# Optimization experiments

Measured on AMD Instinct MI355X. Metric: run time of the kernel, lower is better.

The kernel has to match this reference:

```python
import jax, jax.numpy as jnp
import numpy as np

B, N, P = 16, 128, 4096          # images, proposals/img, pairs/img
D_IN, D_HID = 1024, 512          # input_dim, hidden_dim
D_GEO, D_EMB = 128, 200          # geometry_feat_dim, embed_dim
N_OBJ, N_REL = 151, 51           # obj classes, rel classes (out_dim = 50)
OUT = N_REL - 1
LN_EPS = 1e-5


def _ln(x, g, b):
    mu = jnp.mean(x, axis=-1, keepdims=True)
    var = jnp.var(x, axis=-1, keepdims=True)
    return (x - mu) * jax.lax.rsqrt(var + LN_EPS) * g + b


def setup_inputs() -> dict:
    key = jax.random.key(0)
    ks = jax.random.split(key, 20)
    w = lambda k, shape: (jax.random.normal(k, shape, jnp.float32) * 0.02)
    return {
        'visual_feat': jax.random.normal(ks[0], (B * P, D_IN), jnp.float32),
        'box_info': jax.random.uniform(ks[1], (B, N, 9), jnp.float32),
        'pred_logits': jax.random.normal(ks[2], (B, N, N_OBJ), jnp.float32),
        'pair_idx': jax.random.randint(ks[3], (B, P, 2), 0, N, jnp.int32),
        'obj_sem_w': w(ks[4], (N_OBJ, D_EMB)),
        'pos_w1': w(ks[5], (9, D_GEO)), 'pos_b1': jnp.zeros((D_GEO,), jnp.float32),
        'pos_w2': w(ks[6], (D_GEO, D_GEO)), 'pos_b2': jnp.zeros((D_GEO,), jnp.float32),
        'vis_w': w(ks[7], (D_IN, D_HID)), 'vis_b': jnp.zeros((D_HID,), jnp.float32),
        'geo_w': w(ks[8], (2 * D_EMB + 2 * D_GEO, D_HID)), 'geo_b': jnp.zeros((D_HID,), jnp.float32),
        'fus_g': jnp.ones((2 * D_HID,), jnp.float32), 'fus_bt': jnp.zeros((2 * D_HID,), jnp.float32),
        'fus_w': w(ks[9], (2 * D_HID, D_HID)), 'fus_b': jnp.zeros((D_HID,), jnp.float32),
        'cls_g': jnp.ones((D_HID,), jnp.float32), 'cls_bt': jnp.zeros((D_HID,), jnp.float32),
        'cls_w': w(ks[10], (D_HID, OUT)), 'cls_b': jnp.zeros((OUT,), jnp.float32),
    }


def reference(visual_feat, box_info, pred_logits, pair_idx,
              obj_sem_w, pos_w1, pos_b1, pos_w2, pos_b2,
              vis_w, vis_b, geo_w, geo_b,
              fus_g, fus_bt, fus_w, fus_b,
              cls_g, cls_bt, cls_w, cls_b):
    # detach() in torch -> stop_gradient
    vf = jax.lax.stop_gradient(visual_feat)
    pl = jax.lax.stop_gradient(pred_logits)
    # vis_embed = Sequential(ReLU, Linear): [B*P, D_IN] -> [B, P, D_HID]
    vis = (jnp.maximum(vf, 0.0) @ vis_w + vis_b).reshape(B, P, D_HID)
    # obj_pos_embed = Linear, ReLU, Linear: [B, N, 9] -> [B, N, D_GEO]
    pos = jnp.maximum(box_info @ pos_w1 + pos_b1, 0.0) @ pos_w2 + pos_b2
    # semantic embed: softmax over obj classes @ embedding table -> [B, N, D_EMB]
    sem = jax.nn.softmax(pl, axis=-1) @ obj_sem_w
    bidx = jnp.arange(B)[:, None]
    s, o = pair_idx[..., 0], pair_idx[..., 1]
    # gather pair reps: [B, P, 2*(D_GEO+D_EMB)]
    rep = jnp.concatenate([pos[bidx, s], sem[bidx, s], pos[bidx, o], sem[bidx, o]], axis=-1)
    # proposal_box_feat_extract = Sequential(ReLU, Linear)
    geo = jnp.maximum(rep, 0.0) @ geo_w + geo_b
    # proposal_feat_fusion = Sequential(LayerNorm, ReLU, Linear)
    fused = jnp.concatenate([vis, geo], axis=-1)
    fused = jnp.maximum(_ln(fused, fus_g, fus_bt), 0.0) @ fus_w + fus_b
    # proposal_relness_cls_fc = Sequential(LayerNorm, ReLU, Linear)
    logits = jnp.maximum(_ln(fused, cls_g, cls_bt), 0.0) @ cls_w + cls_b  # [B, P, OUT]
    # predictor_type == 'single': scatter max sigmoid score into NxN matrix
    scores = jnp.max(jax.nn.sigmoid(logits), axis=-1)  # [B, P]
    rel_mat = jnp.zeros((B, N, N), logits.dtype).at[bidx, s, o].set(scores)
    return logits.reshape(B * P, OUT), rel_mat
```

## Files before the change

kernel.cpp:

```cpp
#include <hip/hip_runtime.h>
#include <cstdint>

#define B_    16
#define N_    128
#define P_    4096
#define M_    65536
#define DIN   1024
#define DHID  512
#define DGEO  128
#define DEMB  200
#define NODEF 328
#define NOBJ  151
#define OUTC  50
#define KGEO  656
#define KGEOP 672

typedef __attribute__((ext_vector_type(8))) short bf16x8;
typedef __attribute__((ext_vector_type(4))) float f32x4;

typedef __attribute__((address_space(3))) unsigned char lds_u8;
typedef __attribute__((address_space(1))) unsigned char glb_u8;

static __device__ __forceinline__ void async_copy16(const void* g, void* l) {
  __builtin_amdgcn_global_load_lds((const glb_u8*)g, (lds_u8*)l, 16, 0, 0);
}

static __device__ __forceinline__ unsigned short f2b(float f) {
  union { float f; unsigned u; } v; v.f = f;
  unsigned r = v.u + 0x7fffu + ((v.u >> 16) & 1u);
  return (unsigned short)(r >> 16);
}
static __device__ __forceinline__ float b2f(unsigned short b) {
  union { unsigned u; float f; } v; v.u = ((unsigned)b) << 16;
  return v.f;
}
static __device__ __forceinline__ unsigned pack2(float a, float b) {
  return (unsigned)f2b(a) | ((unsigned)f2b(b) << 16);
}
static __device__ __forceinline__ void unpack8(uint4 raw, float* x) {
  x[0] = b2f(raw.x & 0xffffu); x[1] = b2f(raw.x >> 16);
  x[2] = b2f(raw.y & 0xffffu); x[3] = b2f(raw.y >> 16);
  x[4] = b2f(raw.z & 0xffffu); x[5] = b2f(raw.z >> 16);
  x[6] = b2f(raw.w & 0xffffu); x[7] = b2f(raw.w >> 16);
}

#define ZN   131072
#define TV   (512 * 1024)
#define TG   (512 * KGEOP)
#define TF   (512 * 1024)
#define TC   (128 * 512)
#define PREP_TOT (ZN + TV + TG + TF + TC)
__global__ __launch_bounds__(256)
void prep_kernel(uint4* __restrict__ scat,
                 const float* __restrict__ vis_w, unsigned short* __restrict__ wT_vis,
                 const float* __restrict__ geo_w, unsigned short* __restrict__ wT_geo,
                 const float* __restrict__ fus_w, unsigned short* __restrict__ wT_fus,
                 const float* __restrict__ cls_w, unsigned short* __restrict__ wT_cls) {
  int idx = blockIdx.x * 256 + threadIdx.x;
  if (idx < ZN) { scat[idx] = make_uint4(0, 0, 0, 0); return; }
  idx -= ZN;
  if (idx < TV) {
    int n = idx >> 10, k = idx & 1023;
    wT_vis[idx] = f2b(vis_w[(size_t)k * 512 + n]);
    return;
  }
  idx -= TV;
  if (idx < TG) {
    int n = idx / KGEOP, k = idx - n * KGEOP;
    wT_geo[idx] = (k < KGEO) ? f2b(geo_w[(size_t)k * 512 + n]) : 0;
    return;
  }
  idx -= TG;
  if (idx < TF) {
    int n = idx >> 10, k = idx & 1023;
    wT_fus[idx] = f2b(fus_w[(size_t)k * 512 + n]);
    return;
  }
  idx -= TF;
  if (idx < TC) {
    int n = idx >> 9, k = idx & 511;
    wT_cls[idx] = (n < OUTC) ? f2b(cls_w[(size_t)k * OUTC + n]) : 0;
  }
}

__global__ __launch_bounds__(128)
void node_kernel(const float* __restrict__ box, const float* __restrict__ plog,
                 const float* __restrict__ semw,
                 const float* __restrict__ w1, const float* __restrict__ b1,
                 const float* __restrict__ w2, const float* __restrict__ b2,
                 unsigned short* __restrict__ nodeFb) {
  const int node = blockIdx.x;
  const int t = threadIdx.x;
  __shared__ float sBox[9];
  __shared__ float sH[128];
  __shared__ float sE[NOBJ];
  __shared__ float sRed[4];
  if (t < 9) sBox[t] = box[node * 9 + t];
  float l0 = (t < NOBJ) ? plog[node * NOBJ + t] : -1e30f;
  float l1 = (t + 128 < NOBJ) ? plog[node * NOBJ + t + 128] : -1e30f;
  __syncthreads();
  float h = b1[t];
#pragma unroll
  for (int i = 0; i < 9; i++) h = fmaf(sBox[i], w1[i * 128 + t], h);
  h = fmaxf(h, 0.f);
  sH[t] = h;
  float mx = fmaxf(l0, l1);
#pragma unroll
  for (int off = 32; off >= 1; off >>= 1) mx = fmaxf(mx, __shfl_xor(mx, off));
  if ((t & 63) == 0) sRed[t >> 6] = mx;
  __syncthreads();
  mx = fmaxf(sRed[0], sRed[1]);
  float e0 = (t < NOBJ) ? expf(l0 - mx) : 0.f;
  float e1 = (t + 128 < NOBJ) ? expf(l1 - mx) : 0.f;
  if (t < NOBJ) sE[t] = e0;
  if (t + 128 < NOBJ) sE[t + 128] = e1;
  float sm = e0 + e1;
#pragma unroll
  for (int off = 32; off >= 1; off >>= 1) sm += __shfl_xor(sm, off);
  if ((t & 63) == 0) sRed[2 + (t >> 6)] = sm;
  __syncthreads();
  const float inv = 1.f / (sRed[2] + sRed[3]);
  float pv = b2[t];
  for (int i = 0; i < 128; i++) pv = fmaf(sH[i], w2[i * 128 + t], pv);
  nodeFb[(size_t)node * NODEF + t] = f2b(fmaxf(pv, 0.f));
  float a0 = 0.f, a1 = 0.f;
  const int d1 = (t + 128 < DEMB) ? (t + 128) : 0;
  for (int i = 0; i < NOBJ; i++) {
    float e = sE[i];
    a0 = fmaf(e, semw[i * DEMB + t], a0);
    a1 = fmaf(e, semw[i * DEMB + d1], a1);
  }
  nodeFb[(size_t)node * NODEF + 128 + t] = f2b(fmaxf(a0 * inv, 0.f));
  if (t + 128 < DEMB) nodeFb[(size_t)node * NODEF + 128 + t + 128] = f2b(fmaxf(a1 * inv, 0.f));
}

template<int D>
__global__ __launch_bounds__(256)
void ln_relu_kernel(unsigned short* __restrict__ X,
                    const float* __restrict__ g, const float* __restrict__ bta) {
  constexpr int C = D / 64;
  const int lane = threadIdx.x & 63, wv = threadIdx.x >> 6;
  const size_t row = (size_t)blockIdx.x * 4 + wv;
  unsigned short* xp = X + row * D + lane * C;
  float x[C];
#pragma unroll
  for (int c = 0; c < C; c += 8) {
    uint4 raw = *(const uint4*)(xp + c);
    unpack8(raw, x + c);
  }
  float s = 0.f, s2 = 0.f;
#pragma unroll
  for (int q = 0; q < C; q++) { s += x[q]; s2 = fmaf(x[q], x[q], s2); }
#pragma unroll
  for (int off = 32; off >= 1; off >>= 1) { s += __shfl_xor(s, off); s2 += __shfl_xor(s2, off); }
  const float mu = s / D;
  const float rs = rsqrtf(s2 / D - mu * mu + 1e-5f);
  const float* gp = g + lane * C;
  const float* bp = bta + lane * C;
#pragma unroll
  for (int c = 0; c < C; c += 8) {
    float4 g0 = *(const float4*)(gp + c), g1 = *(const float4*)(gp + c + 4);
    float4 t0 = *(const float4*)(bp + c), t1 = *(const float4*)(bp + c + 4);
    float y0 = fmaxf(fmaf((x[c + 0] - mu) * rs, g0.x, t0.x), 0.f);
    float y1 = fmaxf(fmaf((x[c + 1] - mu) * rs, g0.y, t0.y), 0.f);
    float y2 = fmaxf(fmaf((x[c + 2] - mu) * rs, g0.z, t0.z), 0.f);
    float y3 = fmaxf(fmaf((x[c + 3] - mu) * rs, g0.w, t0.w), 0.f);
    float y4 = fmaxf(fmaf((x[c + 4] - mu) * rs, g1.x, t1.x), 0.f);
    float y5 = fmaxf(fmaf((x[c + 5] - mu) * rs, g1.y, t1.y), 0.f);
    float y6 = fmaxf(fmaf((x[c + 6] - mu) * rs, g1.z, t1.z), 0.f);
    float y7 = fmaxf(fmaf((x[c + 7] - mu) * rs, g1.w, t1.w), 0.f);
    uint4 u;
    u.x = pack2(y0, y1); u.y = pack2(y2, y3);
    u.z = pack2(y4, y5); u.w = pack2(y6, y7);
    *(uint4*)(xp + c) = u;
  }
}

static __device__ __forceinline__ int pair_swz(int bid, int nwg) {
  const int cpx2 = nwg >> 4;
  const int pr = bid >> 1, q = bid & 1;
  return (((pr & 7) * cpx2) + (pr >> 3)) * 2 + q;
}

template<int MODE>
__global__ __launch_bounds__(512)
void gemm256r(const unsigned short* __restrict__ A, int ldaE,
              const unsigned short* __restrict__ Bt, int ldbE,
              const float* __restrict__ bias,
              unsigned short* __restrict__ C, int ldcE, int ccol0,
              int NS, int NBN,
              const int* __restrict__ pidx,
              const unsigned short* __restrict__ nodeFb,
              const unsigned short* __restrict__ zsrc) {
  __shared__ __align__(16) unsigned char smem[131072];
  const int tid = threadIdx.x;
  const int lane = tid & 63, w = tid >> 6;
  const int swz = pair_swz(blockIdx.x, gridDim.x);
  const int bm = swz / NBN, bn = swz - bm * NBN;

  const int sslot = (tid & 3) ^ ((tid >> 3) & 3);
  const int srow = tid >> 2;
  const size_t ldaBy = (size_t)ldaE * 2, ldbBy = (size_t)ldbE * 2;
  const unsigned char* aG = (const unsigned char*)A + (size_t)(bm * 256 + srow) * ldaBy + sslot * 16;
  const unsigned char* bG = (const unsigned char*)Bt + (size_t)(bn * 256 + srow) * ldbBy + sslot * 16;

  const unsigned short* nbS[2];
  const unsigned short* nbO[2];
  if (MODE == 1) {
#pragma unroll
    for (int r = 0; r < 2; r++) {
      int pr = bm * 256 + r * 128 + srow;
      int2 so = *(const int2*)(pidx + 2 * pr);
      int b = pr >> 12;
      nbS[r] = nodeFb + (size_t)((b << 7) + so.x) * NODEF;
      nbO[r] = nodeFb + (size_t)((b << 7) + so.y) * NODEF;
    }
  }

  auto stage = [&](int s) {
    const int slot = s & 3;
    unsigned char* la = smem + slot * 16384 + w * 1024;
    unsigned char* lb = smem + 65536 + slot * 16384 + w * 1024;
    if (MODE == 0) {
      const unsigned char* sa = aG + (size_t)s * 64;
      async_copy16(sa, la);
      async_copy16(sa + 128 * ldaBy, la + 8192);
    } else {
      const int e = s * 32 + sslot * 8;
#pragma unroll
      for (int r = 0; r < 2; r++) {
        uintptr_t ps = (uintptr_t)(nbS[r] + e);
        uintptr_t po = (uintptr_t)(nbO[r] + (e - NODEF));
        uintptr_t pz = (uintptr_t)zsrc;
        uintptr_t sel = (e < NODEF) ? ps : ((e < KGEO) ? po : pz);
        async_copy16((const void*)sel, la + r * 8192);
      }
    }
    const unsigned char* sb = bG + (size_t)s * 64;
    async_copy16(sb, lb);
    async_copy16(sb + 128 * ldbBy, lb + 8192);
  };

  const int wm = w >> 2, wn = w & 3;
  const int frow = lane & 15;
  const int colb = (((lane >> 4) ^ ((frow >> 1) & 3)) << 4);
  const int aRowB = (wm * 128 + frow) * 64;
  const int bRowB = (wn * 64 + frow) * 64;

  f32x4 acc[8][4];
#pragma unroll
  for (int m = 0; m < 8; m++)
#pragma unroll
    for (int n = 0; n < 4; n++) acc[m][n] = (f32x4){0.f, 0.f, 0.f, 0.f};

  stage(0); stage(1); stage(2);
  for (int s = 0; s < NS; ++s) {
    if (s == NS - 1)      asm volatile("s_waitcnt vmcnt(0)" ::: "memory");
    else if (s == NS - 2) asm volatile("s_waitcnt vmcnt(4)" ::: "memory");
    else                  asm volatile("s_waitcnt vmcnt(8)" ::: "memory");
    __builtin_amdgcn_s_barrier();
    __builtin_amdgcn_sched_barrier(0);
    if (s + 3 < NS) stage(s + 3);
    const unsigned char* ab = smem + (s & 3) * 16384;
    const unsigned char* bb = smem + 65536 + (s & 3) * 16384;
    bf16x8 af[8], bfv[4];
#pragma unroll
    for (int m = 0; m < 8; m++) af[m] = *(const bf16x8*)(ab + aRowB + m * 1024 + colb);
#pragma unroll
    for (int n = 0; n < 4; n++) bfv[n] = *(const bf16x8*)(bb + bRowB + n * 1024 + colb);
    __builtin_amdgcn_s_setprio(1);
#pragma unroll
    for (int m = 0; m < 8; m++)
#pragma unroll
      for (int n = 0; n < 4; n++)
        acc[m][n] = __builtin_amdgcn_mfma_f32_16x16x32_bf16(af[m], bfv[n], acc[m][n], 0, 0, 0);
    __builtin_amdgcn_s_setprio(0);
    __builtin_amdgcn_sched_barrier(0);
  }
  const int rb = bm * 256 + wm * 128 + ((lane >> 4) << 2);
  const int cb = bn * 256 + wn * 64 + frow;
#pragma unroll
  for (int n = 0; n < 4; n++) {
    const int col = cb + n * 16;
    const float bv = bias[col];
#pragma unroll
    for (int m = 0; m < 8; m++)
#pragma unroll
      for (int i = 0; i < 4; i++) {
        const int row = rb + m * 16 + i;
        C[(size_t)row * ldcE + ccol0 + col] = f2b(acc[m][n][i] + bv);
      }
  }
}

__global__ __launch_bounds__(512, 4)
void gemm256f3(const float* __restrict__ A,
               const unsigned short* __restrict__ Bt,
               const float* __restrict__ bias,
               unsigned short* __restrict__ C, int ldcE, int ccol0,
               int NBN) {
  constexpr int NS = 32;
  __shared__ __align__(16) unsigned char smem[49152];
  const int tid = threadIdx.x;
  const int lane = tid & 63, w = tid >> 6;
  const int swz = pair_swz(blockIdx.x, gridDim.x);
  const int bm = swz / NBN, bn = swz - bm * NBN;

  const int sslot = (tid & 3) ^ ((tid >> 3) & 3);
  const int srow = tid >> 2;
  const float* aG = A + (size_t)(bm * 128 + srow) * 1024 + sslot * 8;
  const unsigned char* bG = (const unsigned char*)Bt + (size_t)(bn * 256 + srow) * 2048 + sslot * 16;
  unsigned char* laBase = smem + srow * 64 + (tid & 3) * 16;
  unsigned char* lbBase = smem + 16384 + w * 1024;

  uint4 ra0[2], ra1[2];

  auto issueA = [&](int s, uint4* ra) {
    const float* p0 = aG + (size_t)s * 32;
    ra[0] = *(const uint4*)(p0);
    ra[1] = *(const uint4*)(p0 + 4);
  };
  auto issueB = [&](int s) {
    const int slot = s & 1;
    const unsigned char* sb = bG + (size_t)s * 64;
    async_copy16(sb, lbBase + slot * 16384);
    async_copy16(sb + 128 * 2048, lbBase + slot * 16384 + 8192);
  };
  auto writeA = [&](int s, const uint4* ra) {
    const int slot = s & 1;
    float x0 = fmaxf(__uint_as_float(ra[0].x), 0.f);
    float x1 = fmaxf(__uint_as_float(ra[0].y), 0.f);
    float x2 = fmaxf(__uint_as_float(ra[0].z), 0.f);
    float x3 = fmaxf(__uint_as_float(ra[0].w), 0.f);
    float x4 = fmaxf(__uint_as_float(ra[1].x), 0.f);
    float x5 = fmaxf(__uint_as_float(ra[1].y), 0.f);
    float x6 = fmaxf(__uint_as_float(ra[1].z), 0.f);
    float x7 = fmaxf(__uint_as_float(ra[1].w), 0.f);
    uint4 u;
    u.x = pack2(x0, x1); u.y = pack2(x2, x3);
    u.z = pack2(x4, x5); u.w = pack2(x6, x7);
    *(uint4*)(laBase + slot * 8192) = u;
  };

  const int wm = w >> 2, wn = w & 3;
  const int frow = lane & 15;
  const int colb = (((lane >> 4) ^ ((frow >> 1) & 3)) << 4);
  const int aRowB = (wm * 64 + frow) * 64;
  const int bRowB = (wn * 64 + frow) * 64;

  f32x4 acc[4][4];
#pragma unroll
  for (int m = 0; m < 4; m++)
#pragma unroll
    for (int n = 0; n < 4; n++) acc[m][n] = (f32x4){0.f, 0.f, 0.f, 0.f};

  issueA(0, ra0); issueB(0);
  issueA(1, ra1); issueB(1);

#pragma unroll 1
  for (int s = 0; s < NS; s += 2) {
#pragma unroll
    for (int half = 0; half < 2; half++) {
      const int sc = s + half;
      uint4* raC = half ? ra1 : ra0;
      if (sc == NS - 1) asm volatile("s_waitcnt vmcnt(0)" ::: "memory");
      else              asm volatile("s_waitcnt vmcnt(4)" ::: "memory");
      __builtin_amdgcn_sched_barrier(0);
      writeA(sc, raC);
      if (sc + 2 < NS) issueA(sc + 2, raC);
      asm volatile("s_waitcnt lgkmcnt(0)" ::: "memory");
      __builtin_amdgcn_s_barrier();
      __builtin_amdgcn_sched_barrier(0);
      const unsigned char* ab = smem + (sc & 1) * 8192;
      const unsigned char* bb = smem + 16384 + (sc & 1) * 16384;
      bf16x8 af[4];
#pragma unroll
      for (int m = 0; m < 4; m++) af[m] = *(const bf16x8*)(ab + aRowB + m * 1024 + colb);
      __builtin_amdgcn_s_setprio(1);
#pragma unroll
      for (int n = 0; n < 4; n++) {
        bf16x8 bf = *(const bf16x8*)(bb + bRowB + n * 1024 + colb);
#pragma unroll
        for (int m = 0; m < 4; m++)
          acc[m][n] = __builtin_amdgcn_mfma_f32_16x16x32_bf16(af[m], bf, acc[m][n], 0, 0, 0);
      }
      __builtin_amdgcn_s_setprio(0);
      __builtin_amdgcn_sched_barrier(0);
      __builtin_amdgcn_s_barrier();
      __builtin_amdgcn_sched_barrier(0);
      if (sc + 2 < NS) issueB(sc + 2);
    }
  }
  const int rb = bm * 128 + wm * 64 + ((lane >> 4) << 2);
  const int cb = bn * 256 + wn * 64 + frow;
#pragma unroll
  for (int n = 0; n < 4; n++) {
    const int col = cb + n * 16;
    const float bv = bias[col];
#pragma unroll
    for (int m = 0; m < 4; m++)
#pragma unroll
      for (int i = 0; i < 4; i++) {
        const int row = rb + m * 16 + i;
        C[(size_t)row * ldcE + ccol0 + col] = f2b(acc[m][n][i] + bv);
      }
  }
}

__global__ __launch_bounds__(256)
void gemm_cls(const unsigned short* __restrict__ A, int lda,
              const unsigned short* __restrict__ Bt,
              const float* __restrict__ bias,
              float* __restrict__ C,
              int Ktot,
              const int* __restrict__ pidx,
              unsigned long long* __restrict__ scat) {
  __shared__ unsigned short ldsA[128 * 64];
  __shared__ unsigned short ldsB[128 * 64];
  const int tid = threadIdx.x;
  const int lane = tid & 63, wid = tid >> 6;
  const int cpx = gridDim.x >> 3;
  const int bm = (blockIdx.x & 7) * cpx + (blockIdx.x >> 3);

  const int srow = wid * 32 + (lane >> 3);
  const int skof = (lane & 7) * 8;
  const unsigned short* ag = A + (size_t)(bm * 128 + srow) * lda + skof;
  const unsigned short* bg = Bt + (size_t)srow * Ktot + skof;

  f32x4 acc[4][4];
#pragma unroll
  for (int m = 0; m < 4; m++)
#pragma unroll
    for (int n = 0; n < 4; n++) acc[m][n] = (f32x4){0.f, 0.f, 0.f, 0.f};

  const int wm = wid >> 1, wn = wid & 1;
  const int frow = lane & 15;
  const int kgrp = (lane >> 4) << 3;

  for (int kt = 0; kt < Ktot; kt += 64) {
#pragma unroll
    for (int i = 0; i < 4; i++) {
      async_copy16(ag + (size_t)i * 8 * lda + kt, &ldsA[wid * 2048 + i * 512]);
      async_copy16(bg + (size_t)i * 8 * Ktot + kt, &ldsB[wid * 2048 + i * 512]);
    }
    __syncthreads();
#pragma unroll
    for (int kk = 0; kk < 64; kk += 32) {
      bf16x8 af[4], bfr[4];
#pragma unroll
      for (int m = 0; m < 4; m++)
        af[m] = *(const bf16x8*)&ldsA[(wm * 64 + m * 16 + frow) * 64 + kk + kgrp];
#pragma unroll
      for (int n = 0; n < 4; n++)
        bfr[n] = *(const bf16x8*)&ldsB[(wn * 64 + n * 16 + frow) * 64 + kk + kgrp];
#pragma unroll
      for (int m = 0; m < 4; m++)
#pragma unroll
        for (int n = 0; n < 4; n++)
          acc[m][n] = __builtin_amdgcn_mfma_f32_16x16x32_bf16(af[m], bfr[n], acc[m][n], 0, 0, 0);
    }
    __syncthreads();
  }
  const int rb = bm * 128 + wm * 64 + ((lane >> 4) << 2);
#pragma unroll
  for (int n = 0; n < 4; n++) {
    const int col = wn * 64 + frow + n * 16;
    const float bv = (col < OUTC) ? bias[col] : 0.f;
#pragma unroll
    for (int m = 0; m < 4; m++)
#pragma unroll
      for (int i = 0; i < 4; i++) {
        const int row = rb + m * 16 + i;
        if (col < OUTC) C[(size_t)row * OUTC + col] = acc[m][n][i] + bv;
      }
  }
  if (wn == 0) {
#pragma unroll
    for (int m = 0; m < 4; m++)
#pragma unroll
      for (int i = 0; i < 4; i++) {
        float mx = -1e30f;
#pragma unroll
        for (int n = 0; n < 4; n++) {
          const int col = n * 16 + frow;
          float v = acc[m][n][i] + ((col < OUTC) ? bias[col] : 0.f);
          if (col < OUTC) mx = fmaxf(mx, v);
        }
        mx = fmaxf(mx, __shfl_xor(mx, 1));
        mx = fmaxf(mx, __shfl_xor(mx, 2));
        mx = fmaxf(mx, __shfl_xor(mx, 4));
        mx = fmaxf(mx, __shfl_xor(mx, 8));
        if (frow == 0) {
          const int row = rb + m * 16 + i;
          float sc = 1.f / (1.f + expf(-mx));
          int b = row >> 12, p = row & 4095;
          int s = pidx[2 * row], o = pidx[2 * row + 1];
          unsigned long long key = (((unsigned long long)(p + 1)) << 32) |
                                   (unsigned long long)__float_as_uint(sc);
          atomicMax(&scat[((size_t)(b * N_ + s) << 7) + o], key);
        }
      }
  }
}

__global__ void relmat_kernel(const unsigned long long* __restrict__ scat, float* __restrict__ out) {
  int i = blockIdx.x * blockDim.x + threadIdx.x;
  if (i >= B_ * N_ * N_) return;
  unsigned long long v = scat[i];
  out[i] = v ? __uint_as_float((unsigned)(v & 0xffffffffu)) : 0.f;
}

extern "C" void kernel_launch(void* const* d_in, const int* in_sizes, int n_in,
                              void* d_out, int out_size, void* d_ws, size_t ws_size,
                              hipStream_t stream) {
  const float* visual_feat = (const float*)d_in[0];
  const float* box_info    = (const float*)d_in[1];
  const float* pred_logits = (const float*)d_in[2];
  const int*   pair_idx    = (const int*)d_in[3];
  const float* obj_sem_w   = (const float*)d_in[4];
  const float* pos_w1 = (const float*)d_in[5];
  const float* pos_b1 = (const float*)d_in[6];
  const float* pos_w2 = (const float*)d_in[7];
  const float* pos_b2 = (const float*)d_in[8];
  const float* vis_w  = (const float*)d_in[9];
  const float* vis_b  = (const float*)d_in[10];
  const float* geo_w  = (const float*)d_in[11];
  const float* geo_b  = (const float*)d_in[12];
  const float* fus_g  = (const float*)d_in[13];
  const float* fus_bt = (const float*)d_in[14];
  const float* fus_w  = (const float*)d_in[15];
  const float* fus_b  = (const float*)d_in[16];
  const float* cls_g  = (const float*)d_in[17];
  const float* cls_bt = (const float*)d_in[18];
  const float* cls_w  = (const float*)d_in[19];
  const float* cls_b  = (const float*)d_in[20];

  char* ws = (char*)d_ws;
  size_t off = 0;
  auto alloc = [&](size_t bytes) { char* p = ws + off; off += (bytes + 255) & ~(size_t)255; return p; };
  unsigned short* fused = (unsigned short*)alloc((size_t)M_ * 1024 * 2);
  unsigned short* fused2 = (unsigned short*)alloc((size_t)M_ * 512 * 2);
  unsigned short* nodeFb = (unsigned short*)alloc((size_t)B_ * N_ * NODEF * 2);
  unsigned short* wT_vis = (unsigned short*)alloc((size_t)512 * 1024 * 2);
  unsigned short* wT_geo = (unsigned short*)alloc((size_t)512 * KGEOP * 2);
  unsigned short* wT_fus = (unsigned short*)alloc((size_t)512 * 1024 * 2);
  unsigned short* wT_cls = (unsigned short*)alloc((size_t)128 * 512 * 2);
  unsigned long long* scat = (unsigned long long*)alloc((size_t)B_ * N_ * N_ * 8);

  float* out_logits = (float*)d_out;
  float* out_rel = out_logits + (size_t)M_ * OUTC;

  prep_kernel<<<dim3((PREP_TOT + 255) / 256), 256, 0, stream>>>(
      (uint4*)scat, vis_w, wT_vis, geo_w, wT_geo, fus_w, wT_fus, cls_w, wT_cls);
  node_kernel<<<dim3(B_ * N_), 128, 0, stream>>>(box_info, pred_logits, obj_sem_w,
                                                 pos_w1, pos_b1, pos_w2, pos_b2, nodeFb);
  gemm256r<1><<<dim3(512), 512, 0, stream>>>(nullptr, 0, wT_geo, KGEOP, geo_b,
                                             fused, 1024, 512, KGEOP / 32, 2,
                                             pair_idx, nodeFb, (const unsigned short*)scat);
  gemm256f3<<<dim3(1024), 512, 0, stream>>>(visual_feat, wT_vis, vis_b,
                                            fused, 1024, 0, 2);
  ln_relu_kernel<1024><<<dim3(M_ / 4), 256, 0, stream>>>(fused, fus_g, fus_bt);
  gemm256r<0><<<dim3(512), 512, 0, stream>>>(fused, 1024, wT_fus, 1024, fus_b,
                                             fused2, 512, 0, 1024 / 32, 2,
                                             nullptr, nullptr, nullptr);
  ln_relu_kernel<512><<<dim3(M_ / 4), 256, 0, stream>>>(fused2, cls_g, cls_bt);
  gemm_cls<<<dim3(512), 256, 0, stream>>>(fused2, 512, wT_cls, cls_b,
                                          out_logits, 512, pair_idx, scat);
  relmat_kernel<<<dim3((B_ * N_ * N_) / 256), 256, 0, stream>>>(scat, out_rel);
}
```

Before: 429.6 us.

## Shrink bf16 GEMM tile to 128x256 with double buffering for higher occupancy

```diff
diff --git a/kernel.cpp b/kernel.cpp
--- a/kernel.cpp
+++ b/kernel.cpp
@@ -183,16 +183,16 @@
 }
 
 template<int MODE>
-__global__ __launch_bounds__(512)
-void gemm256r(const unsigned short* __restrict__ A, int ldaE,
-              const unsigned short* __restrict__ Bt, int ldbE,
-              const float* __restrict__ bias,
-              unsigned short* __restrict__ C, int ldcE, int ccol0,
-              int NS, int NBN,
-              const int* __restrict__ pidx,
-              const unsigned short* __restrict__ nodeFb,
-              const unsigned short* __restrict__ zsrc) {
-  __shared__ __align__(16) unsigned char smem[131072];
+__global__ __launch_bounds__(512, 4)
+void gemm128x256g(const unsigned short* __restrict__ A, int ldaE,
+                  const unsigned short* __restrict__ Bt, int Ktot,
+                  const float* __restrict__ bias,
+                  unsigned short* __restrict__ C, int ldcE, int ccol0,
+                  int NS, int NBN,
+                  const int* __restrict__ pidx,
+                  const unsigned short* __restrict__ nodeFb,
+                  const unsigned short* __restrict__ zsrc) {
+  __shared__ __align__(16) unsigned char smem[49152];
   const int tid = threadIdx.x;
   const int lane = tid & 63, w = tid >> 6;
   const int swz = pair_swz(blockIdx.x, gridDim.x);
@@ -200,41 +200,32 @@
 
   const int sslot = (tid & 3) ^ ((tid >> 3) & 3);
   const int srow = tid >> 2;
-  const size_t ldaBy = (size_t)ldaE * 2, ldbBy = (size_t)ldbE * 2;
-  const unsigned char* aG = (const unsigned char*)A + (size_t)(bm * 256 + srow) * ldaBy + sslot * 16;
+  const size_t ldaBy = (size_t)ldaE * 2, ldbBy = (size_t)Ktot * 2;
+  const unsigned char* aG = (const unsigned char*)A + (size_t)(bm * 128 + srow) * ldaBy + sslot * 16;
   const unsigned char* bG = (const unsigned char*)Bt + (size_t)(bn * 256 + srow) * ldbBy + sslot * 16;
 
-  const unsigned short* nbS[2];
-  const unsigned short* nbO[2];
-  if (MODE == 1) {
-#pragma unroll
-    for (int r = 0; r < 2; r++) {
-      int pr = bm * 256 + r * 128 + srow;
-      int2 so = *(const int2*)(pidx + 2 * pr);
-      int b = pr >> 12;
-      nbS[r] = nodeFb + (size_t)((b << 7) + so.x) * NODEF;
-      nbO[r] = nodeFb + (size_t)((b << 7) + so.y) * NODEF;
-    }
+  const unsigned short* nbS = nullptr;
+  const unsigned short* nbO = nullptr;
+  if (MODE == 2) {
+    int pr = bm * 128 + srow;
+    int2 so = *(const int2*)(pidx + 2 * pr);
+    int b = pr >> 12;
+    nbS = nodeFb + (size_t)((b << 7) + so.x) * NODEF;
+    nbO = nodeFb + (size_t)((b << 7) + so.y) * NODEF;
   }
 
   auto stage = [&](int s) {
-    const int slot = s & 3;
-    unsigned char* la = smem + slot * 16384 + w * 1024;
-    unsigned char* lb = smem + 65536 + slot * 16384 + w * 1024;
+    const int slot = s & 1;
+    unsigned char* la = smem + slot * 8192 + w * 1024;
+    unsigned char* lb = smem + 16384 + slot * 16384 + w * 1024;
     if (MODE == 0) {
-      const unsigned char* sa = aG + (size_t)s * 64;
-      async_copy16(sa, la);
-      async_copy16(sa + 128 * ldaBy, la + 8192);
+      async_copy16(aG + (size_t)s * 64, la);
     } else {
       const int e = s * 32 + sslot * 8;
-#pragma unroll
-      for (int r = 0; r < 2; r++) {
-        uintptr_t ps = (uintptr_t)(nbS[r] + e);
-        uintptr_t po = (uintptr_t)(nbO[r] + (e - NODEF));
-        uintptr_t pz = (uintptr_t)zsrc;
-        uintptr_t sel = (e < NODEF) ? ps : ((e < KGEO) ? po : pz);
-        async_copy16((const void*)sel, la + r * 8192);
-      }
+      uintptr_t sel = (e < NODEF) ? (uintptr_t)(nbS + e)
+                    : (e < KGEO)  ? (uintptr_t)(nbO + (e - NODEF))
+                                  : (uintptr_t)zsrc;
+      async_copy16((const void*)sel, la);
     }
     const unsigned char* sb = bG + (size_t)s * 64;
     async_copy16(sb, lb);
@@ -244,47 +235,49 @@
   const int wm = w >> 2, wn = w & 3;
   const int frow = lane & 15;
   const int colb = (((lane >> 4) ^ ((frow >> 1) & 3)) << 4);
-  const int aRowB = (wm * 128 + frow) * 64;
+  const int aRowB = (wm * 64 + frow) * 64;
   const int bRowB = (wn * 64 + frow) * 64;
 
-  f32x4 acc[8][4];
-#pragma unroll
-  for (int m = 0; m < 8; m++)
+  f32x4 acc[4][4];
+#pragma unroll
+  for (int m = 0; m < 4; m++)
 #pragma unroll
     for (int n = 0; n < 4; n++) acc[m][n] = (f32x4){0.f, 0.f, 0.f, 0.f};
 
-  stage(0); stage(1); stage(2);
+  stage(0); stage(1);
+#pragma unroll 1
   for (int s = 0; s < NS; ++s) {
-    if (s == NS - 1)      asm volatile("s_waitcnt vmcnt(0)" ::: "memory");
-    else if (s == NS - 2) asm volatile("s_waitcnt vmcnt(4)" ::: "memory");
-    else                  asm volatile("s_waitcnt vmcnt(8)" ::: "memory");
+    if (s == NS - 1) asm volatile("s_waitcnt vmcnt(0)" ::: "memory");
+    else             asm volatile("s_waitcnt vmcnt(3)" ::: "memory");
     __builtin_amdgcn_s_barrier();
     __builtin_amdgcn_sched_barrier(0);
-    if (s + 3 < NS) stage(s + 3);
-    const unsigned char* ab = smem + (s & 3) * 16384;
-    const unsigned char* bb = smem + 65536 + (s & 3) * 16384;
-    bf16x8 af[8], bfv[4];
-#pragma unroll
-    for (int m = 0; m < 8; m++) af[m] = *(const bf16x8*)(ab + aRowB + m * 1024 + colb);
-#pragma unroll
-    for (int n = 0; n < 4; n++) bfv[n] = *(const bf16x8*)(bb + bRowB + n * 1024 + colb);
+    const unsigned char* ab = smem + (s & 1) * 8192;
+    const unsigned char* bb = smem + 16384 + (s & 1) * 16384;
+    bf16x8 af[4];
+#pragma unroll
+    for (int m = 0; m < 4; m++) af[m] = *(const bf16x8*)(ab + aRowB + m * 1024 + colb);
     __builtin_amdgcn_s_setprio(1);
 #pragma unroll
-    for (int m = 0; m < 8; m++)
-#pragma unroll
-      for (int n = 0; n < 4; n++)
-        acc[m][n] = __builtin_amdgcn_mfma_f32_16x16x32_bf16(af[m], bfv[n], acc[m][n], 0, 0, 0);
+    for (int n = 0; n < 4; n++) {
+      bf16x8 bf = *(const bf16x8*)(bb + bRowB + n * 1024 + colb);
+#pragma unroll
+      for (int m = 0; m < 4; m++)
+        acc[m][n] = __builtin_amdgcn_mfma_f32_16x16x32_bf16(af[m], bf, acc[m][n], 0, 0, 0);
+    }
     __builtin_amdgcn_s_setprio(0);
     __builtin_amdgcn_sched_barrier(0);
-  }
-  const int rb = bm * 256 + wm * 128 + ((lane >> 4) << 2);
+    __builtin_amdgcn_s_barrier();
+    __builtin_amdgcn_sched_barrier(0);
+    if (s + 2 < NS) stage(s + 2);
+  }
+  const int rb = bm * 128 + wm * 64 + ((lane >> 4) << 2);
   const int cb = bn * 256 + wn * 64 + frow;
 #pragma unroll
   for (int n = 0; n < 4; n++) {
     const int col = cb + n * 16;
     const float bv = bias[col];
 #pragma unroll
-    for (int m = 0; m < 8; m++)
+    for (int m = 0; m < 4; m++)
 #pragma unroll
       for (int i = 0; i < 4; i++) {
         const int row = rb + m * 16 + i;
@@ -554,15 +547,15 @@
       (uint4*)scat, vis_w, wT_vis, geo_w, wT_geo, fus_w, wT_fus, cls_w, wT_cls);
   node_kernel<<<dim3(B_ * N_), 128, 0, stream>>>(box_info, pred_logits, obj_sem_w,
                                                  pos_w1, pos_b1, pos_w2, pos_b2, nodeFb);
-  gemm256r<1><<<dim3(512), 512, 0, stream>>>(nullptr, 0, wT_geo, KGEOP, geo_b,
-                                             fused, 1024, 512, KGEOP / 32, 2,
-                                             pair_idx, nodeFb, (const unsigned short*)scat);
+  gemm128x256g<2><<<dim3(1024), 512, 0, stream>>>(nullptr, 0, wT_geo, KGEOP, geo_b,
+                                                  fused, 1024, 512, KGEOP / 32, 2,
+                                                  pair_idx, nodeFb, (const unsigned short*)scat);
   gemm256f3<<<dim3(1024), 512, 0, stream>>>(visual_feat, wT_vis, vis_b,
                                             fused, 1024, 0, 2);
   ln_relu_kernel<1024><<<dim3(M_ / 4), 256, 0, stream>>>(fused, fus_g, fus_bt);
-  gemm256r<0><<<dim3(512), 512, 0, stream>>>(fused, 1024, wT_fus, 1024, fus_b,
-                                             fused2, 512, 0, 1024 / 32, 2,
-                                             nullptr, nullptr, nullptr);
+  gemm128x256g<0><<<dim3(1024), 512, 0, stream>>>(fused, 1024, wT_fus, 1024, fus_b,
+                                                  fused2, 512, 0, 1024 / 32, 2,
+                                                  nullptr, nullptr, nullptr);
   ln_relu_kernel<512><<<dim3(M_ / 4), 256, 0, stream>>>(fused2, cls_g, cls_bt);
   gemm_cls<<<dim3(512), 256, 0, stream>>>(fused2, 512, wT_cls, cls_b,
                                           out_logits, 512, pair_idx, scat);
```

Measured after the change: 413.0 us. 3.9% less time.
